# Optimization experiments

Hardware: AMD Instinct MI355X
Metric: run time of the kernel (lower is better)

The kernel has to match this reference:

```python
import jax, jax.numpy as jnp
import numpy as np

B, S, T = 1024, 1024, 32  # batch, seq_len, num_tags


def setup_inputs() -> dict:
    key = jax.random.key(0)
    k1, k2, k3, k4 = jax.random.split(key, 4)
    logits = jax.random.normal(k1, (B, S, T), dtype=jnp.float32)
    transitions = jax.random.normal(k2, (T, T), dtype=jnp.float32)
    tags = jax.random.randint(k3, (B, S), 0, T)
    lengths = jax.random.randint(k4, (B,), 1, S + 1)
    return {"logits": logits, "transitions": transitions, "tags": tags, "lengths": lengths}


def _forward_alg(logits, transitions):
    # viterbi_0 = logits[:, 0, :]; then for t>=1:
    # v_next[b, j] = logsumexp_i(v[b, i] + trans[i, j]) + logits[b, t, j]
    v0 = logits[:, 0, :]  # (B, T)
    emits = jnp.swapaxes(logits[:, 1:, :], 0, 1)  # (S-1, B, T)

    def step(v, emit_t):
        v_next = jax.nn.logsumexp(v[:, :, None] + transitions[None, :, :], axis=1) + emit_t
        return v_next, None

    v_final, _ = jax.lax.scan(step, v0, emits)
    return jax.nn.logsumexp(v_final, axis=1)  # (B,)


def _score_sentence(logits, transitions, tags, lengths):
    # emission scores of gold tags, masked to t < length (note: original ignores
    # lengths in the forward algorithm but uses them here, faithfully reproduced)
    emit = jnp.take_along_axis(logits, tags[:, :, None], axis=2)[..., 0]  # (B, S)
    pos = jnp.arange(S)
    emit_mask = (pos[None, :] < lengths[:, None]).astype(logits.dtype)
    score = jnp.sum(emit * emit_mask, axis=1)
    # transition scores trans[tags[t-1], tags[t]] for 1 <= t < length
    trans_sc = transitions[tags[:, :-1], tags[:, 1:]]  # (B, S-1)
    trans_mask = (pos[None, 1:] < lengths[:, None]).astype(logits.dtype)
    score = score + jnp.sum(trans_sc * trans_mask, axis=1)
    return score  # (B,)


def reference(logits, transitions, tags, lengths):
    log_z = _forward_alg(logits, transitions)
    gold = _score_sentence(logits, transitions, tags, lengths)
    return jnp.mean(log_z - gold)
```

## Files before the change

### kernel.cpp

```cpp
#include <hip/hip_runtime.h>

#define NB 1024
#define NS 1024
#define NT 32
#define L2E 1.44269504088896340736f
#define LN2 0.69314718055994530942f

typedef short        bfrag  __attribute__((ext_vector_type(8)));
typedef float        cfrag  __attribute__((ext_vector_type(16)));
typedef __bf16       bf16x2 __attribute__((ext_vector_type(2)));
typedef float        f32x8  __attribute__((ext_vector_type(8)));
typedef float        f32x4  __attribute__((ext_vector_type(4)));
typedef float        f32x2  __attribute__((ext_vector_type(2)));
typedef unsigned int u32;
typedef unsigned int u32x4  __attribute__((ext_vector_type(4)));

__device__ __forceinline__ float fexp2(float x){ return __builtin_amdgcn_exp2f(x); }
__device__ __forceinline__ float flog2(float x){ return __builtin_amdgcn_logf(x); }

__device__ __forceinline__ u32 pkbf_rne(float a, float b){
    f32x2 t; t.x = a; t.y = b;
    return __builtin_bit_cast(u32, __builtin_convertvector(t, bf16x2));
}
__device__ __forceinline__ u32 pkbf_t(float a, float b){
    return __builtin_amdgcn_perm(__builtin_bit_cast(u32, b),
                                 __builtin_bit_cast(u32, a), 0x07060302u);
}
__device__ __forceinline__ bfrag mk_afrag(f32x8 v){
    u32x4 r;
    r[0] = pkbf_rne(v[0], v[1]); r[1] = pkbf_rne(v[2], v[3]);
    r[2] = pkbf_rne(v[4], v[5]); r[3] = pkbf_rne(v[6], v[7]);
    return __builtin_bit_cast(bfrag, r);
}
__device__ __forceinline__ float ubf(u32 x, int lo){
    return __builtin_bit_cast(float, lo ? (x & 0xFFFF0000u) : (x << 16));
}
__device__ __forceinline__ int exref(float ref){
    u32 xb = __builtin_bit_cast(u32, ref);
    u32 xf = __builtin_amdgcn_readfirstlane(xb);
    int ex = (int)((xf >> 23) & 0xFFu) - 127;
    return ex < -120 ? -120 : (ex > 120 ? 120 : ex);
}

__device__ __forceinline__ int rho(int k){
    int bb = (k >> 2) & 3;
    return (bb == 1 || bb == 2) ? (k ^ 12) : k;
}

template<int N> struct ic { static constexpr int value = N; };
union accu { cfrag c; f32x2 p[8]; };
union q4u  { f32x4 v; f32x2 p[2]; };

__global__ __launch_bounds__(256, 8) void crf_chunk(
    const float* __restrict__ logits, const float* __restrict__ trans,
    const int* __restrict__ tags, const int* __restrict__ lens,
    u32* __restrict__ wmat, float* __restrict__ woff,
    float* __restrict__ gpart, float* __restrict__ outz)
{
    __shared__ __align__(16) float dscall[4 * 512];

    const int tid = threadIdx.x;
    const int wv  = tid >> 6, lt = tid & 63;
    const int m   = lt & 31,  h  = lt >> 5;
    const int bc  = blockIdx.x * 4 + wv;
    const int b   = bc >> 3,  c  = bc & 7;
    float* dsc = dscall + wv * 512;

    if (blockIdx.x == 0 && tid == 0) *outz = 0.0f;

    const float* base = logits + (size_t)b * NS * NT;
    const int    len  = lens[b];
    const int    tb   = b * NS;

    f32x8 Et0, Et1;
    #pragma unroll
    for (int j = 0; j < 8; j++){
        Et0[j] = fexp2(L2E * trans[rho(     8*h + j)*NT + m]);
        Et1[j] = fexp2(L2E * trans[rho(16 + 8*h + j)*NT + m]);
    }
    const bfrag A0f = mk_afrag(Et0);
    const bfrag A1f = mk_afrag(Et1);

    u32x4 B0v, B1v;
    #pragma unroll
    for (int d = 0; d < 4; d++){
        int k0 = 8*h + 2*d;      u32 v = 0;
        if (rho(k0)     == m) v |= 0x3F80u;
        if (rho(k0 + 1) == m) v |= 0x3F800000u;
        B0v[d] = v;
        int k1 = 16 + 8*h + 2*d; v = 0;
        if (rho(k1)     == m) v |= 0x3F80u;
        if (rho(k1 + 1) == m) v |= 0x3F800000u;
        B1v[d] = v;
    }

    cfrag zacc;
    #pragma unroll
    for (int q = 0; q < 16; q++) zacc[q] = 0.0f;

    int   offi = 0;
    float exf  = 0.0f;
    const int tbeg = c*128 + 1;

    float eA[4], eB[4];

    auto issue = [&](float (&e)[4], int k){
        const int t0 = tbeg + k*8 + 4*h;
        #pragma unroll
        for (int i = 0; i < 4; i++){
            int t = t0 + i; t = t > (NS-1) ? (NS-1) : t;
            e[i] = base[t*NT + m];
        }
    };
    auto commit = [&](float (&e)[4], int k){
        float* sp = dsc + (k & 1)*256 + (4*h)*32 + m;
        float a0 = (h == 0) ? -exf : 0.0f;
        sp[0]    = fexp2(fmaf(L2E, e[0], a0));
        sp[32]   = fexp2(L2E * e[1]);
        sp[64]   = fexp2(L2E * e[2]);
        sp[96]   = fexp2(L2E * e[3]);
    };

    auto procN = [&](int k, bool defer, auto nstc){
        constexpr int NST = decltype(nstc)::value;
        const float* db = dsc + (k & 1)*256 + 4*h;
        #pragma unroll
        for (int i = 0; i < NST; i++){
            accu acc;
            acc.c = __builtin_amdgcn_mfma_f32_32x32x16_bf16(
                        A0f, __builtin_bit_cast(bfrag, B0v), zacc, 0, 0, 0);
            acc.c = __builtin_amdgcn_mfma_f32_32x32x16_bf16(
                        A1f, __builtin_bit_cast(bfrag, B1v), acc.c, 0, 0, 0);

            q4u d0, d1, d2, d3;
            d0.v = *(const f32x4*)(db + i*32 +  0);
            d1.v = *(const f32x4*)(db + i*32 +  8);
            d2.v = *(const f32x4*)(db + i*32 + 16);
            d3.v = *(const f32x4*)(db + i*32 + 24);
            acc.p[0] *= d0.p[0]; acc.p[1] *= d0.p[1];
            acc.p[2] *= d1.p[0]; acc.p[3] *= d1.p[1];
            acc.p[4] *= d2.p[0]; acc.p[5] *= d2.p[1];
            acc.p[6] *= d3.p[0]; acc.p[7] *= d3.p[1];

            if (i == 3){
                int ex = exref(fmaxf(acc.c[0], acc.c[8]));
                offi += ex;
                f32x2 s2;
                s2.x = s2.y = __builtin_bit_cast(float, (u32)(127 - ex) << 23);
                #pragma unroll
                for (int q = 0; q < 8; q++) acc.p[q] *= s2;
            }
            if (i == 7 && defer){
                int ex = exref(fmaxf(acc.c[0], acc.c[8]));
                offi += ex;
                exf = (float)ex;
            }

            B0v[0] = pkbf_t(acc.c[0],  acc.c[1]);  B0v[1] = pkbf_t(acc.c[2],  acc.c[3]);
            B0v[2] = pkbf_t(acc.c[4],  acc.c[5]);  B0v[3] = pkbf_t(acc.c[6],  acc.c[7]);
            B1v[0] = pkbf_t(acc.c[8],  acc.c[9]);  B1v[1] = pkbf_t(acc.c[10], acc.c[11]);
            B1v[2] = pkbf_t(acc.c[12], acc.c[13]); B1v[3] = pkbf_t(acc.c[14], acc.c[15]);
        }
    };

    issue(eA, 0); commit(eA, 0);
    #pragma unroll 1
    for (int k = 0; k < 14; k += 2){
        issue(eB, k + 1);
        procN(k, true, ic<8>{});
        commit(eB, k + 1);
        issue(eA, k + 2);
        procN(k + 1, true, ic<8>{});
        commit(eA, k + 2);
    }
    issue(eB, 15);
    procN(14, true, ic<8>{});
    commit(eB, 15);
    if (c != 7) procN(15, false, ic<8>{});
    else        procN(15, false, ic<7>{});

    const size_t mb = (size_t)bc * 512;
    #pragma unroll
    for (int d = 0; d < 4; d++){
        wmat[mb + d*64 + lt]     = B0v[d];
        wmat[mb + (4+d)*64 + lt] = B1v[d];
    }
    if (lt == 0) woff[bc] = (float)offi;

    {
        const int t1 = tbeg + 2*lt;
        const int t2 = t1 + 1;
        const int i2 = t2 > (NS-1) ? (NS-1) : t2;
        const int g0 = tags[tb + t1 - 1];
        const int g1 = tags[tb + t1];
        const int g2 = tags[tb + i2];
        float gg = 0.0f;
        if (t1 < len) gg += base[t1*NT + g1] + trans[g0*NT + g1];
        if (t2 < len) gg += base[t2*NT + g2] + trans[g1*NT + g2];
        #pragma unroll
        for (int d = 1; d < 64; d <<= 1) gg += __shfl_xor(gg, d, 64);
        if (lt == 0){
            if (c == 0) gg += base[tags[tb]];
            gpart[bc] = gg;
        }
    }
}

__global__ __launch_bounds__(64) void crf_combine(
    const float* __restrict__ logits, const int* __restrict__ tags,
    const u32* __restrict__ wmat, const float* __restrict__ woff,
    const float* __restrict__ gpart, float* __restrict__ out)
{
    const int lt = threadIdx.x;
    const int b  = blockIdx.x;
    const float* base = logits + (size_t)b * NS * NT;

    float4 gp0 = ((const float4*)(gpart + b*8))[0];
    float4 gp1 = ((const float4*)(gpart + b*8))[1];
    const float gold = (gp0.x + gp0.y) + (gp0.z + gp0.w)
                     + (gp1.x + gp1.y) + (gp1.z + gp1.w);

    float offs[8];
    #pragma unroll
    for (int cc = 0; cc < 8; cc++) offs[cc] = woff[b*8 + cc];

    const int n   = lt & 31;
    const int bb2 = (n >> 2) & 3;
    const int nn  = (bb2 == 1 || bb2 == 2) ? (n ^ 12) : n;
    const int segbase = (nn >> 4)*256 + ((nn >> 3) & 1)*32 + ((nn >> 1) & 3)*64;
    const int lo  = nn & 1;
    const u32* wbm = wmat + (size_t)b * 8 * 512 + segbase;

    float v    = fexp2(L2E * base[n]);
    float voff = 0.0f;

    uint4 mdA[8], mdB[8];
    {
        const uint4* mp = (const uint4*)(wbm);
        #pragma unroll
        for (int qq = 0; qq < 8; qq++) mdA[qq] = mp[qq];
    }

    #pragma unroll
    for (int cc = 0; cc < 8; cc++){
        uint4 (&cur)[8] = (cc & 1) ? mdB : mdA;
        uint4 (&nxt)[8] = (cc & 1) ? mdA : mdB;
        if (cc < 7){
            const uint4* mp = (const uint4*)(wbm + (cc + 1)*512);
            #pragma unroll
            for (int qq = 0; qq < 8; qq++) nxt[qq] = mp[qq];
        }

        float acc = 0.0f;
        #pragma unroll
        for (int qq = 0; qq < 8; qq++){
            float u0 = __shfl(v, 4*qq + 0, 64);
            float u1 = __shfl(v, 4*qq + 1, 64);
            float u2 = __shfl(v, 4*qq + 2, 64);
            float u3 = __shfl(v, 4*qq + 3, 64);
            acc = fmaf(ubf(cur[qq].x, lo), u0, acc);
            acc = fmaf(ubf(cur[qq].y, lo), u1, acc);
            acc = fmaf(ubf(cur[qq].z, lo), u2, acc);
            acc = fmaf(ubf(cur[qq].w, lo), u3, acc);
        }
        float mx = acc;
        #pragma unroll
        for (int d = 1; d <= 16; d <<= 1) mx = fmaxf(mx, __shfl_xor(mx, d, 64));
        int ex = exref(mx);
        v = acc * __builtin_bit_cast(float, (u32)(127 - ex) << 23);
        voff += (float)ex + offs[cc];
    }

    float s = v;
    #pragma unroll
    for (int d = 1; d <= 16; d <<= 1) s += __shfl_xor(s, d, 64);

    if (lt == 0){
        float logz = LN2 * (voff + flog2(s));
        atomicAdd(out, (logz - gold) * (1.0f / (float)NB));
    }
}

extern "C" void kernel_launch(void* const* d_in, const int* in_sizes, int n_in,
                              void* d_out, int out_size, void* d_ws, size_t ws_size,
                              hipStream_t stream) {
    const float* logits = (const float*)d_in[0];
    const float* trans  = (const float*)d_in[1];
    const int*   tags   = (const int*)d_in[2];
    const int*   lens   = (const int*)d_in[3];

    u32*   wmat  = (u32*)d_ws;
    float* woff  = (float*)((char*)d_ws + 16u*1024u*1024u);
    float* gpart = woff + 8192;

    crf_chunk  <<<2048, 256, 0, stream>>>(logits, trans, tags, lens,
                                          wmat, woff, gpart, (float*)d_out);
    crf_combine<<<1024,  64, 0, stream>>>(logits, tags, wmat, woff, gpart,
                                          (float*)d_out);
}
```

Baseline: 252.4 us.

## Combine chunk transfer matrices with MFMA products in 4-wave blocks

```diff
diff --git a/kernel.cpp b/kernel.cpp
--- a/kernel.cpp
+++ b/kernel.cpp
@@ -31,9 +31,6 @@
     r[0] = pkbf_rne(v[0], v[1]); r[1] = pkbf_rne(v[2], v[3]);
     r[2] = pkbf_rne(v[4], v[5]); r[3] = pkbf_rne(v[6], v[7]);
     return __builtin_bit_cast(bfrag, r);
-}
-__device__ __forceinline__ float ubf(u32 x, int lo){
-    return __builtin_bit_cast(float, lo ? (x & 0xFFFF0000u) : (x << 16));
 }
 __device__ __forceinline__ int exref(float ref){
     u32 xb = __builtin_bit_cast(u32, ref);
@@ -179,11 +176,10 @@
     if (c != 7) procN(15, false, ic<8>{});
     else        procN(15, false, ic<7>{});
 
-    const size_t mb = (size_t)bc * 512;
-    #pragma unroll
-    for (int d = 0; d < 4; d++){
-        wmat[mb + d*64 + lt]     = B0v[d];
-        wmat[mb + (4+d)*64 + lt] = B1v[d];
+    {
+        u32* wp = wmat + (size_t)bc * 512 + (size_t)lt * 8;
+        *(u32x4*)(wp)     = B0v;
+        *(u32x4*)(wp + 4) = B1v;
     }
     if (lt == 0) woff[bc] = (float)offi;
 
@@ -206,74 +202,99 @@
     }
 }
 
-__global__ __launch_bounds__(64) void crf_combine(
-    const float* __restrict__ logits, const int* __restrict__ tags,
+__global__ __launch_bounds__(256) void crf_combine(
+    const float* __restrict__ logits,
     const u32* __restrict__ wmat, const float* __restrict__ woff,
     const float* __restrict__ gpart, float* __restrict__ out)
 {
-    const int lt = threadIdx.x;
-    const int b  = blockIdx.x;
+    const int tid = threadIdx.x;
+    const int wv  = tid >> 6, lt = tid & 63;
+    const int m   = lt & 31,  h  = lt >> 5;
+    const int b   = blockIdx.x * 4 + wv;
     const float* base = logits + (size_t)b * NS * NT;
+
+    uint4 mf[16];
+    const u32* wb = wmat + (size_t)b * 8 * 512 + (size_t)lt * 8;
+    #pragma unroll
+    for (int j = 0; j < 8; j++){
+        mf[2*j]     = *(const uint4*)(wb + j*512);
+        mf[2*j + 1] = *(const uint4*)(wb + j*512 + 4);
+    }
 
     float4 gp0 = ((const float4*)(gpart + b*8))[0];
     float4 gp1 = ((const float4*)(gpart + b*8))[1];
     const float gold = (gp0.x + gp0.y) + (gp0.z + gp0.w)
                      + (gp1.x + gp1.y) + (gp1.z + gp1.w);
 
-    float offs[8];
-    #pragma unroll
-    for (int cc = 0; cc < 8; cc++) offs[cc] = woff[b*8 + cc];
-
-    const int n   = lt & 31;
-    const int bb2 = (n >> 2) & 3;
-    const int nn  = (bb2 == 1 || bb2 == 2) ? (n ^ 12) : n;
-    const int segbase = (nn >> 4)*256 + ((nn >> 3) & 1)*32 + ((nn >> 1) & 3)*64;
-    const int lo  = nn & 1;
-    const u32* wbm = wmat + (size_t)b * 8 * 512 + segbase;
-
-    float v    = fexp2(L2E * base[n]);
     float voff = 0.0f;
-
-    uint4 mdA[8], mdB[8];
-    {
-        const uint4* mp = (const uint4*)(wbm);
-        #pragma unroll
-        for (int qq = 0; qq < 8; qq++) mdA[qq] = mp[qq];
-    }
-
-    #pragma unroll
-    for (int cc = 0; cc < 8; cc++){
-        uint4 (&cur)[8] = (cc & 1) ? mdB : mdA;
-        uint4 (&nxt)[8] = (cc & 1) ? mdA : mdB;
-        if (cc < 7){
-            const uint4* mp = (const uint4*)(wbm + (cc + 1)*512);
-            #pragma unroll
-            for (int qq = 0; qq < 8; qq++) nxt[qq] = mp[qq];
-        }
-
-        float acc = 0.0f;
-        #pragma unroll
-        for (int qq = 0; qq < 8; qq++){
-            float u0 = __shfl(v, 4*qq + 0, 64);
-            float u1 = __shfl(v, 4*qq + 1, 64);
-            float u2 = __shfl(v, 4*qq + 2, 64);
-            float u3 = __shfl(v, 4*qq + 3, 64);
-            acc = fmaf(ubf(cur[qq].x, lo), u0, acc);
-            acc = fmaf(ubf(cur[qq].y, lo), u1, acc);
-            acc = fmaf(ubf(cur[qq].z, lo), u2, acc);
-            acc = fmaf(ubf(cur[qq].w, lo), u3, acc);
-        }
-        float mx = acc;
-        #pragma unroll
-        for (int d = 1; d <= 16; d <<= 1) mx = fmaxf(mx, __shfl_xor(mx, d, 64));
+    #pragma unroll
+    for (int cc = 0; cc < 8; cc++) voff += woff[b*8 + cc];
+
+    u32x4 S0, S1;
+    #pragma unroll
+    for (int d = 0; d < 4; d++){
+        int k0 = 8*h + 2*d;      u32 v = 0;
+        if (rho(k0)     == m) v |= 0x3F80u;
+        if (rho(k0 + 1) == m) v |= 0x3F800000u;
+        S0[d] = v;
+        int k1 = 16 + 8*h + 2*d; v = 0;
+        if (rho(k1)     == m) v |= 0x3F80u;
+        if (rho(k1 + 1) == m) v |= 0x3F800000u;
+        S1[d] = v;
+    }
+
+    cfrag zacc;
+    #pragma unroll
+    for (int q = 0; q < 16; q++) zacc[q] = 0.0f;
+
+    #pragma unroll
+    for (int j = 7; j >= 0; j--){
+        accu acc;
+        acc.c = __builtin_amdgcn_mfma_f32_32x32x16_bf16(
+                    __builtin_bit_cast(bfrag, mf[2*j]),
+                    __builtin_bit_cast(bfrag, S0), zacc, 0, 0, 0);
+        acc.c = __builtin_amdgcn_mfma_f32_32x32x16_bf16(
+                    __builtin_bit_cast(bfrag, mf[2*j + 1]),
+                    __builtin_bit_cast(bfrag, S1), acc.c, 0, 0, 0);
+
+        float mx = acc.c[0];
+        #pragma unroll
+        for (int q = 1; q < 16; q++) mx = fmaxf(mx, acc.c[q]);
+        #pragma unroll
+        for (int d = 1; d < 64; d <<= 1) mx = fmaxf(mx, __shfl_xor(mx, d, 64));
         int ex = exref(mx);
-        v = acc * __builtin_bit_cast(float, (u32)(127 - ex) << 23);
-        voff += (float)ex + offs[cc];
-    }
-
-    float s = v;
-    #pragma unroll
-    for (int d = 1; d <= 16; d <<= 1) s += __shfl_xor(s, d, 64);
+        float sc = __builtin_bit_cast(float, (u32)(127 - ex) << 23);
+        #pragma unroll
+        for (int q = 0; q < 16; q++) acc.c[q] *= sc;
+        voff += (float)ex;
+
+        S0[0] = pkbf_t(acc.c[0],  acc.c[1]);  S0[1] = pkbf_t(acc.c[2],  acc.c[3]);
+        S0[2] = pkbf_t(acc.c[4],  acc.c[5]);  S0[3] = pkbf_t(acc.c[6],  acc.c[7]);
+        S1[0] = pkbf_t(acc.c[8],  acc.c[9]);  S1[1] = pkbf_t(acc.c[10], acc.c[11]);
+        S1[2] = pkbf_t(acc.c[12], acc.c[13]); S1[3] = pkbf_t(acc.c[14], acc.c[15]);
+    }
+
+    u32x4 V0, V1;
+    #pragma unroll
+    for (int d = 0; d < 4; d++){
+        int k0 = 8*h + 2*d;
+        V0[d] = pkbf_rne(fexp2(L2E * base[rho(k0)]), fexp2(L2E * base[rho(k0+1)]));
+        int k1 = 16 + 8*h + 2*d;
+        V1[d] = pkbf_rne(fexp2(L2E * base[rho(k1)]), fexp2(L2E * base[rho(k1+1)]));
+    }
+
+    accu fin;
+    fin.c = __builtin_amdgcn_mfma_f32_32x32x16_bf16(
+                __builtin_bit_cast(bfrag, S0), __builtin_bit_cast(bfrag, V0),
+                zacc, 0, 0, 0);
+    fin.c = __builtin_amdgcn_mfma_f32_32x32x16_bf16(
+                __builtin_bit_cast(bfrag, S1), __builtin_bit_cast(bfrag, V1),
+                fin.c, 0, 0, 0);
+
+    float s = 0.0f;
+    #pragma unroll
+    for (int q = 0; q < 16; q++) s += fin.c[q];
+    s += __shfl_xor(s, 32, 64);
 
     if (lt == 0){
         float logz = LN2 * (voff + flog2(s));
@@ -295,6 +316,6 @@
 
     crf_chunk  <<<2048, 256, 0, stream>>>(logits, trans, tags, lens,
                                           wmat, woff, gpart, (float*)d_out);
-    crf_combine<<<1024,  64, 0, stream>>>(logits, tags, wmat, woff, gpart,
+    crf_combine<<< 256, 256, 0, stream>>>(logits, wmat, woff, gpart,
                                           (float*)d_out);
 }
```

Result: no change. 248.5 us (-1.6%).
